# Performance work log

Hardware: AMD Instinct MI355X
Metric: run time of the kernel (lower is better)

The kernel has to match this reference:

```python
import jax, jax.numpy as jnp
import numpy as np

C = 100000
D = 512
KEEP_RATIO = 0.5
EPS = 1.1920929e-07  # torch.finfo(float32).eps
K = max(1, int(C * KEEP_RATIO))


def _l2norm(x):
    # F.normalize(dim=-1): x / max(||x||, eps)
    n = jnp.linalg.norm(x, axis=-1, keepdims=True)
    return x / jnp.maximum(n, EPS)


def setup_inputs() -> dict:
    key = jax.random.key(0)
    k1, k2, k3 = jax.random.split(key, 3)
    tensor = jax.random.normal(k1, (1024, D), dtype=jnp.float32)
    target = jax.random.randint(k2, (1024,), 0, C, dtype=jnp.int32)
    # xavier_normal_ on (C, D): std = sqrt(2 / (C + D))
    std = np.sqrt(2.0 / (C + D)).astype(np.float32)
    weight = jax.random.normal(k3, (C, D), dtype=jnp.float32) * std
    return {"tensor": tensor, "target": target, "weight": weight}


def reference(tensor, target, weight):
    # --- target mining (no-grad in original) ---
    t_n = _l2norm(tensor)            # (B, D)
    w_n = _l2norm(weight)            # (C, D)
    # max over batch of cosine similarity -> per-class score (C,)
    scores = jnp.max(jnp.einsum("bd,cd->bc", t_n, w_n), axis=0)
    # ground-truth classes always kept
    scores = scores.at[target].set(2.0)
    _, topk_idx = jax.lax.top_k(scores, K)
    subsample = jnp.sort(topk_idx)                       # (K,) ascending
    # remap targets into subsampled index space (targets guaranteed present)
    new_target = jnp.searchsorted(subsample, target).astype(jnp.int32)
    # --- head ---
    w_sub = weight[subsample]                            # (K, D) gather
    logits = jnp.einsum("bd,kd->bk", _l2norm(tensor), _l2norm(w_sub))
    return logits, new_target
```

## Files before the change

### kernel.cpp

```cpp
#include <hip/hip_runtime.h>

#define C_CLS 100000
#define D_DIM 512
#define B_ROWS 1024
#define K_KEEP 50000
#define EPS_F 1.1920929e-07f
#define MB_CT 128
#define BAND 2e-3f
#define DELTA 4e-4f
#define RMAX 32768

typedef short v8s __attribute__((ext_vector_type(8)));
typedef float v4f __attribute__((ext_vector_type(4)));

struct Ctrl { unsigned prefix; unsigned need; };

__device__ __forceinline__ unsigned key_of(float f){
  unsigned u = __float_as_uint(f);
  return (u & 0x80000000u) ? ~u : (u | 0x80000000u);
}
__device__ __forceinline__ float key_inv(unsigned k){
  unsigned u = (k & 0x80000000u) ? (k & 0x7FFFFFFFu) : ~k;
  return __uint_as_float(u);
}
__device__ __forceinline__ unsigned short f2bf_rne(float f){
  unsigned u = __float_as_uint(f);
  unsigned r = (u + 0x7FFFu + ((u >> 16) & 1u)) >> 16;
  return (unsigned short)r;
}
__device__ __forceinline__ float bf2f(unsigned short h){
  return __uint_as_float(((unsigned)h) << 16);
}


__global__ __launch_bounds__(64) void norm_t_kernel(const float* __restrict__ t, float* __restrict__ tn,
                                                    unsigned short* __restrict__ tnph, unsigned short* __restrict__ tnpl,
                                                    const int* __restrict__ tgt, unsigned* __restrict__ keys){
  int row = blockIdx.x, lane = threadIdx.x;
  if (lane == 0) atomicMax(&keys[tgt[row]], key_of(2.0f));
  const float4* p = (const float4*)(t + (size_t)row * D_DIM);
  float4 a = p[lane*2+0], b = p[lane*2+1];
  float s = a.x*a.x + a.y*a.y + a.z*a.z + a.w*a.w
          + b.x*b.x + b.y*b.y + b.z*b.z + b.w*b.w;
  #pragma unroll
  for (int off = 32; off; off >>= 1) s += __shfl_xor(s, off);
  float den = fmaxf(sqrtf(s), EPS_F);
  float o[8] = {a.x/den, a.y/den, a.z/den, a.w/den, b.x/den, b.y/den, b.z/den, b.w/den};
  float4* q = (float4*)(tn + (size_t)row * D_DIM);
  q[lane*2+0] = make_float4(o[0],o[1],o[2],o[3]);
  q[lane*2+1] = make_float4(o[4],o[5],o[6],o[7]);
  v8s hv, lv;
  #pragma unroll
  for (int j = 0; j < 8; ++j){
    unsigned short h = f2bf_rne(o[j]);
    hv[j] = (short)h;
    lv[j] = (short)f2bf_rne(o[j] - bf2f(h));
  }
  size_t di = (size_t)((row & ~15) + (lane >> 2)) * 512 + (lane & 3) * 128 + (row & 15) * 8;
  *(v8s*)(tnph + di) = hv;
  *(v8s*)(tnpl + di) = lv;
}

__device__ __forceinline__ void load_a2(const unsigned short* __restrict__ tp, int b0, int ks, int lane, v8s* dst){
  #pragma unroll
  for (int i = 0; i < 2; ++i){
    int t = b0 + i*16 + (ks >> 5);
    dst[i] = *(const v8s*)(tp + (size_t)t * 512 + lane * 8);
  }
}

__global__ __launch_bounds__(512, 2) void mine_kernel(
    const unsigned short* __restrict__ tnph, const unsigned short* __restrict__ tnpl,
    const float* __restrict__ w, unsigned* __restrict__ keys,
    float* __restrict__ S, float* __restrict__ winv_g){
  __shared__ unsigned short lw[MB_CT * D_DIM];
  __shared__ float wn[MB_CT];
  const int tid = threadIdx.x;
  const int lane = tid & 63;
  const int cb = blockIdx.x * MB_CT;
  #pragma unroll
  for (int st = 0; st < 16; ++st){
    int g = tid + st * 512;
    int row = g >> 6, fc = g & 63;
    int c = cb + row; if (c >= C_CLS) c = C_CLS - 1;
    const float4* src = (const float4*)(w + (size_t)c * D_DIM + fc * 8);
    float4 v0 = src[0], v1 = src[1];
    float vv[8] = {v0.x,v0.y,v0.z,v0.w,v1.x,v1.y,v1.z,v1.w};
    float s = 0.f;
    #pragma unroll
    for (int j = 0; j < 8; ++j) s += vv[j]*vv[j];
    #pragma unroll
    for (int off = 32; off; off >>= 1) s += __shfl_xor(s, off);
    if (lane == 0) wn[row] = 1.0f / fmaxf(sqrtf(s), EPS_F);
    v8s hv;
    #pragma unroll
    for (int j = 0; j < 8; ++j) hv[j] = (short)f2bf_rne(vv[j]);
    int csw = fc ^ (row & 7);
    *(v8s*)&lw[(size_t)row * D_DIM + csw * 8] = hv;
  }
  __syncthreads();
  if (tid < MB_CT && cb + tid < C_CLS) winv_g[cb + tid] = wn[tid];

  const int wv = tid >> 6;
  const int lr = lane & 15, lg = lane >> 4;
  const int bbase = wv * 128;
  float runmax[8] = {-1e30f,-1e30f,-1e30f,-1e30f,-1e30f,-1e30f,-1e30f,-1e30f};
  v4f acc[8][2];
  #pragma unroll
  for (int j = 0; j < 8; ++j)
    #pragma unroll
    for (int i = 0; i < 2; ++i) acc[j][i] = (v4f){0.f,0.f,0.f,0.f};

  v8s cah[2], cal[2];
  load_a2(tnph, bbase, 0, lane, cah);
  load_a2(tnpl, bbase, 0, lane, cal);

  for (int it = 0; it < 64; ++it){
    const int chunk = it >> 4, ks = (it & 15) << 5;
    const int b0 = bbase + chunk * 32;
    v8s nah[2], nal[2];
    if (it < 63){
      int nit = it + 1;
      int nb0 = bbase + (nit >> 4) * 32, nks = (nit & 15) << 5;
      load_a2(tnph, nb0, nks, lane, nah);
      load_a2(tnpl, nb0, nks, lane, nal);
    }
    v8s bh[8];
    #pragma unroll
    for (int j = 0; j < 8; ++j){
      int row = j*16 + lr;
      int ch = ((ks >> 3) + lg) ^ (lr & 7);
      bh[j] = *(const v8s*)&lw[(size_t)row * D_DIM + ch * 8];
    }
    #pragma unroll
    for (int j = 0; j < 8; ++j)
      #pragma unroll
      for (int i = 0; i < 2; ++i){
        acc[j][i] = __builtin_amdgcn_mfma_f32_16x16x32_bf16(cah[i], bh[j], acc[j][i], 0, 0, 0);
        acc[j][i] = __builtin_amdgcn_mfma_f32_16x16x32_bf16(cal[i], bh[j], acc[j][i], 0, 0, 0);
      }
    if ((it & 15) == 15){
      #pragma unroll
      for (int j = 0; j < 8; ++j){
        float m = acc[j][0][0];
        #pragma unroll
        for (int i = 0; i < 2; ++i)
          #pragma unroll
          for (int r = 0; r < 4; ++r) m = fmaxf(m, acc[j][i][r]);
        runmax[j] = fmaxf(runmax[j], m);
        int cls = cb + j*16 + lr;
        if (cls < C_CLS){
          #pragma unroll
          for (int i = 0; i < 2; ++i){
            float4 v = make_float4(acc[j][i][0], acc[j][i][1], acc[j][i][2], acc[j][i][3]);
            *(float4*)(S + (size_t)cls * B_ROWS + b0 + i*16 + lg*4) = v;
          }
        }
        #pragma unroll
        for (int i = 0; i < 2; ++i) acc[j][i] = (v4f){0.f,0.f,0.f,0.f};
      }
    }
    if (it < 63){
      #pragma unroll
      for (int i = 0; i < 2; ++i){ cah[i] = nah[i]; cal[i] = nal[i]; }
    }
  }
  #pragma unroll
  for (int j = 0; j < 8; ++j){
    float m = runmax[j];
    m = fmaxf(m, __shfl_xor(m, 16));
    m = fmaxf(m, __shfl_xor(m, 32));
    int cls = cb + j*16 + lr;
    if (lg == 0 && cls < C_CLS)
      atomicMax(&keys[cls], key_of(m * wn[j*16 + lr]));
  }
}

__global__ __launch_bounds__(256) void histsel_kernel(const unsigned* __restrict__ keys, unsigned* __restrict__ hist,
                                                      unsigned* __restrict__ done, Ctrl* __restrict__ ctrl, int shift){
  __shared__ unsigned h[256];
  __shared__ int lastf;
  int t = threadIdx.x;
  h[t] = 0u;
  __syncthreads();
  unsigned himask = (shift >= 24) ? 0u : (0xFFFFFFFFu << (shift + 8));
  unsigned prefix = (shift == 24) ? 0u : (ctrl->prefix & himask);
  for (int c = blockIdx.x * 256 + t; c < C_CLS; c += gridDim.x * 256){
    unsigned k = keys[c];
    if ((k & himask) == prefix) atomicAdd(&h[(k >> shift) & 255], 1u);
  }
  __syncthreads();
  if (h[t]) atomicAdd(&hist[t], h[t]);
  __threadfence();
  if (t == 0) lastf = (atomicAdd(done, 1u) == (unsigned)(gridDim.x - 1));
  __syncthreads();
  if (lastf){
    unsigned v = __hip_atomic_load(&hist[t], __ATOMIC_RELAXED, __HIP_MEMORY_SCOPE_AGENT);
    h[t] = v;
    __syncthreads();
    if (t == 0){
      unsigned need = (shift == 24) ? (unsigned)K_KEEP : ctrl->need;
      unsigned pfx  = (shift == 24) ? 0u : ctrl->prefix;
      unsigned cum = 0; int b;
      for (b = 255; b >= 0; --b){
        if (cum + h[b] >= need) break;
        cum += h[b];
      }
      if (b < 0) b = 0;
      ctrl->prefix = pfx | ((unsigned)b << shift);
      ctrl->need = need - cum;
      __hip_atomic_store(done, 0u, __ATOMIC_RELAXED, __HIP_MEMORY_SCOPE_AGENT);
    }
    __hip_atomic_store(&hist[t], 0u, __ATOMIC_RELAXED, __HIP_MEMORY_SCOPE_AGENT);
  }
}

__global__ void band_kernel(const unsigned* __restrict__ keys, const Ctrl* __restrict__ ctrl,
                            int* __restrict__ rlist, int* __restrict__ rcount){
  int c = blockIdx.x * 256 + threadIdx.x;
  if (c >= C_CLS) return;
  unsigned k = keys[c];
  if (k == key_of(2.0f)) return;
  float t = key_inv(ctrl->prefix);
  if (fabsf(key_inv(k) - t) <= BAND){
    int i = atomicAdd(rcount, 1);
    if (i < RMAX) rlist[i] = c;
  }
}

__global__ __launch_bounds__(256) void refine_kernel(
    const float* __restrict__ tn, const float* __restrict__ w,
    const float* __restrict__ winv, const float* __restrict__ S,
    const int* __restrict__ rlist, const int* __restrict__ rcount,
    unsigned* __restrict__ keys){
  __shared__ float red[256];
  __shared__ double dred[256];
  __shared__ int cand[32];
  __shared__ int ncand;
  int n = *rcount; if (n > RMAX) n = RMAX;
  int t = threadIdx.x;
  for (int i = blockIdx.x; i < n; i += gridDim.x){
    int c = rlist[i];
    const v4f* srow = (const v4f*)(S + (size_t)c * B_ROWS);
    v4f sv = srow[t];
    float m = fmaxf(fmaxf(sv[0],sv[1]), fmaxf(sv[2],sv[3]));
    red[t] = m; __syncthreads();
    for (int off2 = 128; off2; off2 >>= 1){
      if (t < off2) red[t] = fmaxf(red[t], red[t+off2]);
      __syncthreads();
    }
    float thr = red[0] - DELTA;
    if (t == 0) ncand = 0;
    __syncthreads();
    #pragma unroll
    for (int e = 0; e < 4; ++e){
      if (sv[e] >= thr){
        int ci = atomicAdd(&ncand, 1);
        if (ci < 32) cand[ci] = t*4 + e;
      }
    }
    __syncthreads();
    int nc = ncand; if (nc > 32) nc = 32;
    const float* wrow = w + (size_t)c * D_DIM;
    double w0 = (double)wrow[2*t], w1 = (double)wrow[2*t+1];
    double best = -1e300;
    for (int q = 0; q < nc; ++q){
      int b = cand[q];
      const float* tr = tn + (size_t)b * D_DIM;
      double p = fma((double)tr[2*t], w0, (double)tr[2*t+1] * w1);
      dred[t] = p; __syncthreads();
      for (int off2 = 128; off2; off2 >>= 1){
        if (t < off2) dred[t] += dred[t+off2];
        __syncthreads();
      }
      if (t == 0) best = fmax(best, dred[0]);
      __syncthreads();
    }
    if (t == 0) keys[c] = key_of((float)(best * (double)winv[c]));
    __syncthreads();
  }
}

__global__ __launch_bounds__(256) void scanA_kernel(const unsigned* __restrict__ keys, const Ctrl* __restrict__ ctrl,
                                                    uint2* __restrict__ bsum2, unsigned* __restrict__ done2, int nb){
  __shared__ unsigned red[256];
  __shared__ int lastf;
  int t = threadIdx.x;
  unsigned T = ctrl->prefix;
  int base = blockIdx.x * 1024 + t * 4;
  unsigned pack = 0;
  #pragma unroll
  for (int j = 0; j < 4; ++j){
    int c = base + j;
    if (c < C_CLS){
      unsigned k = keys[c];
      if (k > T) pack += 0x10000u;
      else if (k == T) pack += 1u;
    }
  }
  red[t] = pack; __syncthreads();
  for (int off = 128; off; off >>= 1){
    if (t < off) red[t] += red[t + off];
    __syncthreads();
  }
  if (t == 0) bsum2[blockIdx.x] = make_uint2(red[0] >> 16, red[0] & 0xFFFFu);
  __threadfence();
  if (t == 0) lastf = (atomicAdd(done2, 1u) == (unsigned)(gridDim.x - 1));
  __syncthreads();
  if (lastf && t == 0){
    unsigned rg = 0, re = 0;
    for (int i = 0; i < nb; ++i){
      unsigned vx = __hip_atomic_load(&bsum2[i].x, __ATOMIC_RELAXED, __HIP_MEMORY_SCOPE_AGENT);
      unsigned vy = __hip_atomic_load(&bsum2[i].y, __ATOMIC_RELAXED, __HIP_MEMORY_SCOPE_AGENT);
      __hip_atomic_store(&bsum2[i].x, rg, __ATOMIC_RELAXED, __HIP_MEMORY_SCOPE_AGENT);
      __hip_atomic_store(&bsum2[i].y, re, __ATOMIC_RELAXED, __HIP_MEMORY_SCOPE_AGENT);
      rg += vx; re += vy;
    }
    __hip_atomic_store(done2, 0u, __ATOMIC_RELAXED, __HIP_MEMORY_SCOPE_AGENT);
  }
}

__global__ __launch_bounds__(256) void scanC_kernel(const unsigned* __restrict__ keys, const Ctrl* __restrict__ ctrl,
                                                    const uint2* __restrict__ bsum2, unsigned* __restrict__ pos,
                                                    int* __restrict__ sel){
  __shared__ unsigned ls[256];
  int t = threadIdx.x;
  unsigned T = ctrl->prefix, need = ctrl->need;
  int base = blockIdx.x * 1024 + t * 4;
  unsigned gtv[4], eqv[4], pack = 0;
  #pragma unroll
  for (int j = 0; j < 4; ++j){
    int c = base + j;
    unsigned k = (c < C_CLS) ? keys[c] : 0u;
    gtv[j] = (c < C_CLS && k > T) ? 1u : 0u;
    eqv[j] = (c < C_CLS && k == T) ? 1u : 0u;
    pack += (gtv[j] << 16) + eqv[j];
  }
  ls[t] = pack; __syncthreads();
  for (int off = 1; off < 256; off <<= 1){
    unsigned v = (t >= off) ? ls[t - off] : 0u;
    __syncthreads();
    ls[t] += v;
    __syncthreads();
  }
  unsigned excl = ls[t] - pack;
  uint2 bs = bsum2[blockIdx.x];
  unsigned gtx = bs.x + (excl >> 16);
  unsigned eqx = bs.y + (excl & 0xFFFFu);
  #pragma unroll
  for (int j = 0; j < 4; ++j){
    int c = base + j;
    if (c < C_CLS){
      unsigned p = gtx + (eqx < need ? eqx : need);
      pos[c] = p;
      if (gtv[j] || (eqv[j] && eqx < need)) sel[p] = c;
      gtx += gtv[j]; eqx += eqv[j];
    }
  }
}

__global__ void ntgt_kernel(const int* __restrict__ tgt, const unsigned* __restrict__ pos, float* __restrict__ out){
  int b = blockIdx.x * 256 + threadIdx.x;
  if (b < B_ROWS) out[(size_t)B_ROWS * K_KEEP + b] = (float)pos[tgt[b]];
}

__global__ __launch_bounds__(256) void head_copy_kernel(const float* __restrict__ S, const float* __restrict__ winv,
                                                        const int* __restrict__ sel, float* __restrict__ out){
  __shared__ float tile[64][68];
  __shared__ float wsc[64];
  int k0 = blockIdx.x * 64;
  int b0 = blockIdx.y * 64;
  int tid = threadIdx.x;
  int nk = K_KEEP - k0; if (nk > 64) nk = 64;
  if (tid < 64){
    int kk = k0 + tid;
    wsc[tid] = (kk < K_KEEP) ? winv[sel[kk]] : 0.f;
  }
  int i = tid >> 2, part = tid & 3;
  if (i < nk){
    int c = sel[k0 + i];
    const float4* src = (const float4*)(S + (size_t)c * B_ROWS + b0 + part * 16);
    #pragma unroll
    for (int p = 0; p < 4; ++p)
      *(float4*)&tile[i][part*16 + 4*p] = src[p];
  }
  __syncthreads();
  int bb = tid >> 2, q = tid & 3;
  size_t orow = (size_t)(b0 + bb) * K_KEEP + k0;
  #pragma unroll
  for (int t4 = 0; t4 < 4; ++t4){
    int k = q*16 + t4*4;
    if (k + 3 < nk){
      float4 v = make_float4(tile[k+0][bb]*wsc[k+0], tile[k+1][bb]*wsc[k+1],
                             tile[k+2][bb]*wsc[k+2], tile[k+3][bb]*wsc[k+3]);
      *(float4*)(out + orow + k) = v;
    } else {
      for (int e = 0; e < 4; ++e)
        if (k + e < nk) out[orow + k + e] = tile[k+e][bb]*wsc[k+e];
    }
  }
}

extern "C" void kernel_launch(void* const* d_in, const int* in_sizes, int n_in,
                              void* d_out, int out_size, void* d_ws, size_t ws_size,
                              hipStream_t stream){
  const float* tensor = (const float*)d_in[0];
  const int*   target = (const int*)d_in[1];
  const float* weight = (const float*)d_in[2];
  float* out = (float*)d_out;

  char* ws = (char*)d_ws;
  size_t off = 0;
  auto carve = [&](size_t bytes) -> char* {
    char* p = ws + off;
    off = (off + bytes + 511) & ~(size_t)511;
    return p;
  };
  float*          tn   = (float*)carve((size_t)B_ROWS * D_DIM * 4);
  unsigned short* tnph = (unsigned short*)carve((size_t)B_ROWS * D_DIM * 2);
  unsigned short* tnpl = (unsigned short*)carve((size_t)B_ROWS * D_DIM * 2);
  float*          winv = (float*)carve((size_t)C_CLS * 4);
  size_t zs = off;
  unsigned* keys   = (unsigned*)carve((size_t)C_CLS * 4);
  unsigned* hist   = (unsigned*)carve(256 * 4);
  unsigned* done   = (unsigned*)carve(64);
  unsigned* done2  = (unsigned*)carve(64);
  int*      rcount = (int*)carve(64);
  size_t ze = off;
  Ctrl*     ctrl   = (Ctrl*)carve(64);
  uint2*    bsum2  = (uint2*)carve(128 * 8);
  int*      rlist  = (int*)carve((size_t)RMAX * 4);
  unsigned* pos    = (unsigned*)carve((size_t)C_CLS * 4);
  int*      sel    = (int*)carve((size_t)K_KEEP * 4);
  float*    S      = (float*)carve((size_t)C_CLS * B_ROWS * 4);
  (void)in_sizes; (void)n_in; (void)out_size; (void)ws_size;

  hipMemsetAsync(ws + zs, 0, ze - zs, stream);

  norm_t_kernel<<<B_ROWS, 64, 0, stream>>>(tensor, tn, tnph, tnpl, target, keys);

  mine_kernel<<<(C_CLS + MB_CT - 1) / MB_CT, 512, 0, stream>>>(tnph, tnpl, weight, keys, S, winv);

  for (int shift = 24; shift >= 0; shift -= 8)
    histsel_kernel<<<128, 256, 0, stream>>>(keys, hist, done, ctrl, shift);

  band_kernel<<<(C_CLS + 255) / 256, 256, 0, stream>>>(keys, ctrl, rlist, rcount);
  refine_kernel<<<2048, 256, 0, stream>>>(tn, weight, winv, S, rlist, rcount, keys);

  for (int shift = 24; shift >= 0; shift -= 8)
    histsel_kernel<<<128, 256, 0, stream>>>(keys, hist, done, ctrl, shift);

  const int nb = (C_CLS + 1023) / 1024;
  scanA_kernel<<<nb, 256, 0, stream>>>(keys, ctrl, bsum2, done2, nb);
  scanC_kernel<<<nb, 256, 0, stream>>>(keys, ctrl, bsum2, pos, sel);

  ntgt_kernel<<<(B_ROWS + 255) / 256, 256, 0, stream>>>(target, pos, out);
  head_copy_kernel<<<dim3((K_KEEP + 63) / 64, B_ROWS / 64), 256, 0, stream>>>(S, winv, sel, out);
}
```

Measured before the change: 692.6 us.

## Halve mine tile for higher occupancy and enlarge swizzled head-copy transpose tiles

The mining kernel now processes 64 classes per block instead of 128. That halves its LDS footprint and accumulator registers, so launch bounds can allow 4 blocks per CU instead of 2, aiming at better latency hiding. The head copy kernel moves from 64x64 padded tiles to 128x128 tiles with an XOR-swizzled LDS layout. Each thread now gathers 256-byte contiguous runs from S and writes 64 contiguous output floats. The risks are a 64 KB LDS tile that limits head_copy occupancy, and more mine blocks that each reload the A fragments from global memory.

Measured after the change: 691.8 us. Within noise of the previous version (-0.1%).

```diff
diff --git a/kernel.cpp b/kernel.cpp
--- a/kernel.cpp
+++ b/kernel.cpp
@@ -5,7 +5,7 @@
 #define B_ROWS 1024
 #define K_KEEP 50000
 #define EPS_F 1.1920929e-07f
-#define MB_CT 128
+#define MB_CT 64
 #define BAND 2e-3f
 #define DELTA 4e-4f
 #define RMAX 32768
@@ -69,7 +69,7 @@
   }
 }
 
-__global__ __launch_bounds__(512, 2) void mine_kernel(
+__global__ __launch_bounds__(512, 4) void mine_kernel(
     const unsigned short* __restrict__ tnph, const unsigned short* __restrict__ tnpl,
     const float* __restrict__ w, unsigned* __restrict__ keys,
     float* __restrict__ S, float* __restrict__ winv_g){
@@ -79,7 +79,7 @@
   const int lane = tid & 63;
   const int cb = blockIdx.x * MB_CT;
   #pragma unroll
-  for (int st = 0; st < 16; ++st){
+  for (int st = 0; st < 8; ++st){
     int g = tid + st * 512;
     int row = g >> 6, fc = g & 63;
     int c = cb + row; if (c >= C_CLS) c = C_CLS - 1;
@@ -104,10 +104,10 @@
   const int wv = tid >> 6;
   const int lr = lane & 15, lg = lane >> 4;
   const int bbase = wv * 128;
-  float runmax[8] = {-1e30f,-1e30f,-1e30f,-1e30f,-1e30f,-1e30f,-1e30f,-1e30f};
-  v4f acc[8][2];
-  #pragma unroll
-  for (int j = 0; j < 8; ++j)
+  float runmax[4] = {-1e30f,-1e30f,-1e30f,-1e30f};
+  v4f acc[4][2];
+  #pragma unroll
+  for (int j = 0; j < 4; ++j)
     #pragma unroll
     for (int i = 0; i < 2; ++i) acc[j][i] = (v4f){0.f,0.f,0.f,0.f};
 
@@ -125,15 +125,15 @@
       load_a2(tnph, nb0, nks, lane, nah);
       load_a2(tnpl, nb0, nks, lane, nal);
     }
-    v8s bh[8];
-    #pragma unroll
-    for (int j = 0; j < 8; ++j){
+    v8s bh[4];
+    #pragma unroll
+    for (int j = 0; j < 4; ++j){
       int row = j*16 + lr;
       int ch = ((ks >> 3) + lg) ^ (lr & 7);
       bh[j] = *(const v8s*)&lw[(size_t)row * D_DIM + ch * 8];
     }
     #pragma unroll
-    for (int j = 0; j < 8; ++j)
+    for (int j = 0; j < 4; ++j)
       #pragma unroll
       for (int i = 0; i < 2; ++i){
         acc[j][i] = __builtin_amdgcn_mfma_f32_16x16x32_bf16(cah[i], bh[j], acc[j][i], 0, 0, 0);
@@ -141,7 +141,7 @@
       }
     if ((it & 15) == 15){
       #pragma unroll
-      for (int j = 0; j < 8; ++j){
+      for (int j = 0; j < 4; ++j){
         float m = acc[j][0][0];
         #pragma unroll
         for (int i = 0; i < 2; ++i)
@@ -166,7 +166,7 @@
     }
   }
   #pragma unroll
-  for (int j = 0; j < 8; ++j){
+  for (int j = 0; j < 4; ++j){
     float m = runmax[j];
     m = fmaxf(m, __shfl_xor(m, 16));
     m = fmaxf(m, __shfl_xor(m, 32));
@@ -366,37 +366,45 @@
 
 __global__ __launch_bounds__(256) void head_copy_kernel(const float* __restrict__ S, const float* __restrict__ winv,
                                                         const int* __restrict__ sel, float* __restrict__ out){
-  __shared__ float tile[64][68];
-  __shared__ float wsc[64];
-  int k0 = blockIdx.x * 64;
-  int b0 = blockIdx.y * 64;
+  __shared__ float tile[128 * 128];
+  __shared__ float wsc[128];
+  int k0 = blockIdx.x * 128;
+  int b0 = blockIdx.y * 128;
   int tid = threadIdx.x;
-  int nk = K_KEEP - k0; if (nk > 64) nk = 64;
-  if (tid < 64){
+  int nk = K_KEEP - k0; if (nk > 128) nk = 128;
+  if (tid < 128){
     int kk = k0 + tid;
     wsc[tid] = (kk < K_KEEP) ? winv[sel[kk]] : 0.f;
   }
-  int i = tid >> 2, part = tid & 3;
+  int i = tid >> 1, part = tid & 1;
   if (i < nk){
     int c = sel[k0 + i];
-    const float4* src = (const float4*)(S + (size_t)c * B_ROWS + b0 + part * 16);
-    #pragma unroll
-    for (int p = 0; p < 4; ++p)
-      *(float4*)&tile[i][part*16 + 4*p] = src[p];
-  }
-  __syncthreads();
-  int bb = tid >> 2, q = tid & 3;
-  size_t orow = (size_t)(b0 + bb) * K_KEEP + k0;
-  #pragma unroll
-  for (int t4 = 0; t4 < 4; ++t4){
-    int k = q*16 + t4*4;
+    const float4* src = (const float4*)(S + (size_t)c * B_ROWS + b0) + part * 16;
+    #pragma unroll
+    for (int p = 0; p < 16; ++p){
+      int q = part * 16 + p;
+      int sq = q ^ ((i & 7) << 2);
+      *(float4*)&tile[i * 128 + sq * 4] = src[p];
+    }
+  }
+  __syncthreads();
+  int bb = tid >> 1, half = tid & 1;
+  size_t orow = (size_t)(b0 + bb) * K_KEEP + k0 + half * 64;
+  int kbase = half * 64;
+  int qb = bb >> 2, eb = bb & 3;
+  #pragma unroll
+  for (int p = 0; p < 16; ++p){
+    int k = kbase + 4 * p;
     if (k + 3 < nk){
-      float4 v = make_float4(tile[k+0][bb]*wsc[k+0], tile[k+1][bb]*wsc[k+1],
-                             tile[k+2][bb]*wsc[k+2], tile[k+3][bb]*wsc[k+3]);
-      *(float4*)(out + orow + k) = v;
+      float v0 = tile[(k+0) * 128 + ((qb ^ (((k+0) & 7) << 2)) << 2) + eb] * wsc[k+0];
+      float v1 = tile[(k+1) * 128 + ((qb ^ (((k+1) & 7) << 2)) << 2) + eb] * wsc[k+1];
+      float v2 = tile[(k+2) * 128 + ((qb ^ (((k+2) & 7) << 2)) << 2) + eb] * wsc[k+2];
+      float v3 = tile[(k+3) * 128 + ((qb ^ (((k+3) & 7) << 2)) << 2) + eb] * wsc[k+3];
+      *(float4*)(out + orow + 4 * p) = make_float4(v0, v1, v2, v3);
     } else {
       for (int e = 0; e < 4; ++e)
-        if (k + e < nk) out[orow + k + e] = tile[k+e][bb]*wsc[k+e];
+        if (k + e < nk)
+          out[orow + 4 * p + e] = tile[(k+e) * 128 + ((qb ^ (((k+e) & 7) << 2)) << 2) + eb] * wsc[k+e];
     }
   }
 }
@@ -455,5 +463,5 @@
   scanC_kernel<<<nb, 256, 0, stream>>>(keys, ctrl, bsum2, pos, sel);
 
   ntgt_kernel<<<(B_ROWS + 255) / 256, 256, 0, stream>>>(target, pos, out);
-  head_copy_kernel<<<dim3((K_KEEP + 63) / 64, B_ROWS / 64), 256, 0, stream>>>(S, winv, sel, out);
-}
+  head_copy_kernel<<<dim3((K_KEEP + 127) / 128, B_ROWS / 128), 256, 0, stream>>>(S, winv, sel, out);
+}
```
